# Kernel optimization log

Hardware: AMD Instinct MI355X
Metric: run time of the kernel (lower is better)

Reference implementation:

```python
import jax, jax.numpy as jnp
import numpy as np

N_NODES, FEAT_DIM, EMBED_DIM, BATCH, N_NEIGH = 200000, 128, 64, 8192, 64


def setup_inputs() -> dict:
    key = jax.random.key(0)
    k0, k1, k2, k3, k4, k5 = jax.random.split(key, 6)
    return {
        "features_table": jax.random.normal(k0, (N_NODES, FEAT_DIM), jnp.float32),
        # xavier-uniform-like scale for [2*feat_dim, embed_dim]
        "weight": jax.random.normal(k1, (2 * FEAT_DIM, EMBED_DIM), jnp.float32)
        * (1.0 / np.sqrt(2 * FEAT_DIM)),
        "nodes": jax.random.randint(k2, (BATCH,), 0, N_NODES),
        "batch_scores": jax.random.normal(k3, (BATCH, 2), jnp.float32),
        "neigh_scores": jax.random.normal(k4, (BATCH, N_NEIGH, 2), jnp.float32),
        "neighs_ids": jax.random.randint(k5, (BATCH, N_NEIGH), 0, N_NODES),
        "num_sample": 16,
    }


def reference(features_table, weight, nodes, batch_scores, neigh_scores, neighs_ids, num_sample):
    # |center_score - neigh_score| per candidate neighbor  -> [B, K]
    score_diff = jnp.abs(batch_scores[:, :1] - neigh_scores[:, :, 0])
    # keep num_sample neighbors with SMALLEST score diff (top_k on negated diffs)
    neg_top, sel_idx = jax.lax.top_k(-score_diff, num_sample)  # [B, k]
    samp_scores = -neg_top  # selected (ascending-ish) score diffs, as in choose_step_test
    sel_ids = jnp.take_along_axis(neighs_ids, sel_idx, axis=1)  # [B, k]
    # masked-mean aggregation == mean of the k selected neighbor features
    neigh_feats = features_table[sel_ids]            # [B, k, F]
    agg_feats = neigh_feats.mean(axis=1)             # [B, F]
    self_feats = features_table[nodes]               # [B, F]
    cat_feats = jnp.concatenate([self_feats, agg_feats], axis=1)  # [B, 2F]
    to_feats = jax.nn.relu(cat_feats @ weight)       # [B, E]
    return to_feats, samp_scores
```

## Files before the change

kernel.cpp:

```cpp
#include <hip/hip_runtime.h>

#define BATCH   8192
#define NNEIGH  64
#define FEAT    128
#define EMBED   64
#define ROWS    8
#define CATP    260
#define EPAD    68
#define KCH     8

__global__ __launch_bounds__(256, 4) void intra_agg_kernel(
    const float* __restrict__ feat,
    const float* __restrict__ W,
    const int*   __restrict__ nodes,
    const float* __restrict__ bscore,
    const float* __restrict__ nscore,
    const int*   __restrict__ nids,
    const int*   __restrict__ ns_ptr,
    float*       __restrict__ out)
{
    const int b0   = blockIdx.x * ROWS;
    const int tid  = threadIdx.x;
    const int lane = tid & 63;
    const int wave = tid >> 6;
    const int ns   = *ns_ptr;

    __shared__ float s_cat[ROWS * CATP];
    __shared__ float s_part[KCH][ROWS][EPAD];
    __shared__ float s_diff[ROWS][NNEIGH];

    const int r0   = wave * 2;
    const int half = lane >> 5;
    const int c    = lane & 31;
    const int rA   = b0 + r0;
    const int rB   = rA + 1;

    const int    selfnode = nodes[rA + half];
    const float4 self4    = *(const float4*)&feat[(size_t)selfnode * FEAT + c * 4];
    const int    nidA     = nids[rA * NNEIGH + lane];
    const int    nidB     = nids[rB * NNEIGH + lane];

    const float  ctrA = bscore[rA * 2];
    const float  ctrB = bscore[rB * 2];
    const float2 scA  = *(const float2*)&nscore[(size_t)(rA * NNEIGH + lane) * 2];
    const float2 scB  = *(const float2*)&nscore[(size_t)(rB * NNEIGH + lane) * 2];
    const float  dA   = fabsf(ctrA - scA.x);
    const float  dB   = fabsf(ctrB - scB.x);

    s_diff[r0][lane]     = dA;
    s_diff[r0 + 1][lane] = dB;

    int rankA = 0, rankB = 0;
    {
        const float4* prA = (const float4*)&s_diff[r0][0];
        const float4* prB = (const float4*)&s_diff[r0 + 1][0];
        #pragma unroll
        for (int q = 0; q < 16; ++q) {
            const float4 vA = prA[q];
            const float4 vB = prB[q];
            const int j0 = q * 4;
            rankA += (int)((vA.x < dA) | ((vA.x == dA) & (j0 + 0 < lane)));
            rankA += (int)((vA.y < dA) | ((vA.y == dA) & (j0 + 1 < lane)));
            rankA += (int)((vA.z < dA) | ((vA.z == dA) & (j0 + 2 < lane)));
            rankA += (int)((vA.w < dA) | ((vA.w == dA) & (j0 + 3 < lane)));
            rankB += (int)((vB.x < dB) | ((vB.x == dB) & (j0 + 0 < lane)));
            rankB += (int)((vB.y < dB) | ((vB.y == dB) & (j0 + 1 < lane)));
            rankB += (int)((vB.z < dB) | ((vB.z == dB) & (j0 + 2 < lane)));
            rankB += (int)((vB.w < dB) | ((vB.w == dB) & (j0 + 3 < lane)));
        }
    }

    if (rankA < ns) out[(size_t)BATCH * EMBED + (size_t)rA * ns + rankA] = dA;
    if (rankB < ns) out[(size_t)BATCH * EMBED + (size_t)rB * ns + rankB] = dB;

    const int gidA = __builtin_amdgcn_ds_permute(rankA << 2, nidA);
    const int gidB = __builtin_amdgcn_ds_permute(rankB << 2, nidB);

    float4 a = make_float4(0.f, 0.f, 0.f, 0.f);
    if (ns == 16) {
        #pragma unroll
        for (int j = 0; j < 16; ++j) {
            const int iA = __builtin_amdgcn_readlane(gidA, j);
            const int iB = __builtin_amdgcn_readlane(gidB, j);
            const int id = half ? iB : iA;
            const float4 v = *(const float4*)&feat[(size_t)id * FEAT + c * 4];
            a.x += v.x; a.y += v.y; a.z += v.z; a.w += v.w;
        }
    } else {
        for (int j = 0; j < ns; ++j) {
            const int iA = __builtin_amdgcn_readlane(gidA, j);
            const int iB = __builtin_amdgcn_readlane(gidB, j);
            const int id = half ? iB : iA;
            const float4 v = *(const float4*)&feat[(size_t)id * FEAT + c * 4];
            a.x += v.x; a.y += v.y; a.z += v.z; a.w += v.w;
        }
    }
    const float inv_ns = 1.0f / (float)ns;
    a.x *= inv_ns; a.y *= inv_ns; a.z *= inv_ns; a.w *= inv_ns;

    {
        const int r = r0 + half;
        *(float4*)&s_cat[r * CATP + c * 4]        = self4;
        *(float4*)&s_cat[r * CATP + FEAT + c * 4] = a;
    }
    __syncthreads();

    {
        const int q  = tid & 15;
        const int rq = (tid >> 4) & 1;
        const int ks = tid >> 5;
        const int k0 = ks * 32;

        float4 acc[4];
        #pragma unroll
        for (int r = 0; r < 4; ++r) acc[r] = make_float4(0.f, 0.f, 0.f, 0.f);

        #pragma unroll
        for (int kk = 0; kk < 32; kk += 4) {
            const int k = k0 + kk;
            float4 cv[4];
            #pragma unroll
            for (int r = 0; r < 4; ++r)
                cv[r] = *(const float4*)&s_cat[(rq * 4 + r) * CATP + k];
            #pragma unroll
            for (int t = 0; t < 4; ++t) {
                const float4 w4 = *(const float4*)&W[(size_t)(k + t) * EMBED + q * 4];
                #pragma unroll
                for (int r = 0; r < 4; ++r) {
                    const float cf = (t == 0) ? cv[r].x : (t == 1) ? cv[r].y
                                   : (t == 2) ? cv[r].z : cv[r].w;
                    acc[r].x += cf * w4.x; acc[r].y += cf * w4.y;
                    acc[r].z += cf * w4.z; acc[r].w += cf * w4.w;
                }
            }
        }
        #pragma unroll
        for (int r = 0; r < 4; ++r)
            *(float4*)&s_part[ks][rq * 4 + r][q * 4] = acc[r];
    }
    __syncthreads();

    if (tid < ROWS * 16) {
        const int r2 = tid >> 4;
        const int q  = tid & 15;
        float4 o = make_float4(0.f, 0.f, 0.f, 0.f);
        #pragma unroll
        for (int p = 0; p < KCH; ++p) {
            const float4 v = *(const float4*)&s_part[p][r2][q * 4];
            o.x += v.x; o.y += v.y; o.z += v.z; o.w += v.w;
        }
        o.x = fmaxf(o.x, 0.f); o.y = fmaxf(o.y, 0.f);
        o.z = fmaxf(o.z, 0.f); o.w = fmaxf(o.w, 0.f);
        *(float4*)&out[(size_t)(b0 + r2) * EMBED + q * 4] = o;
    }
}

extern "C" void kernel_launch(void* const* d_in, const int* in_sizes, int n_in,
                              void* d_out, int out_size, void* d_ws, size_t ws_size,
                              hipStream_t stream) {
    const float* feat   = (const float*)d_in[0];
    const float* W      = (const float*)d_in[1];
    const int*   nodes  = (const int*)d_in[2];
    const float* bscore = (const float*)d_in[3];
    const float* nscore = (const float*)d_in[4];
    const int*   nids   = (const int*)d_in[5];
    const int*   nsamp  = (const int*)d_in[6];
    float* out = (float*)d_out;

    intra_agg_kernel<<<BATCH / ROWS, 256, 0, stream>>>(feat, W, nodes, bscore,
                                                       nscore, nids, nsamp, out);
}
```

Measured before the change: 21.94 us.

## Overlap neighbor gathers with self-feature half of the matmul

Stores self features to shared memory early and splits the matmul K range so each thread block computes the self-feature half while the neighbor gathers are in flight, in two batches of 8 loads. The gather loop is hardcoded to 16 neighbors, dropping the general-ns path, and uses raw s_barrier with lgkmcnt waits instead of __syncthreads. It also reorders the K partitioning so each chunk covers 16 self and 16 aggregated columns. The cost is more registers for the 8 buffered float4 loads, and the kernel now gives wrong results if num_sample differs from 16.

```diff
diff --git a/kernel.cpp b/kernel.cpp
--- a/kernel.cpp
+++ b/kernel.cpp
@@ -49,6 +49,12 @@
 
     s_diff[r0][lane]     = dA;
     s_diff[r0 + 1][lane] = dB;
+    {
+        const int r = r0 + half;
+        *(float4*)&s_cat[r * CATP + c * 4] = self4;
+    }
+    asm volatile("s_waitcnt lgkmcnt(0)" ::: "memory");
+    __builtin_amdgcn_s_barrier();
 
     int rankA = 0, rankB = 0;
     {
@@ -70,74 +76,91 @@
         }
     }
 
+    const int gidA = __builtin_amdgcn_ds_permute(rankA << 2, nidA);
+    const int gidB = __builtin_amdgcn_ds_permute(rankB << 2, nidB);
+
+    const int mq  = tid & 15;
+    const int mrq = (tid >> 4) & 1;
+    const int mks = tid >> 5;
+    const int kS  = mks * 16;
+    const int kG  = FEAT + mks * 16;
+
+    float4 acc[4];
+    #pragma unroll
+    for (int r = 0; r < 4; ++r) acc[r] = make_float4(0.f, 0.f, 0.f, 0.f);
+
+#define MM8(kb)                                                               \
+    {                                                                         \
+        _Pragma("unroll")                                                     \
+        for (int kk = 0; kk < 8; kk += 4) {                                   \
+            const int k = (kb) + kk;                                          \
+            float4 cv[4];                                                     \
+            _Pragma("unroll")                                                 \
+            for (int r = 0; r < 4; ++r)                                       \
+                cv[r] = *(const float4*)&s_cat[(mrq * 4 + r) * CATP + k];     \
+            _Pragma("unroll")                                                 \
+            for (int t = 0; t < 4; ++t) {                                     \
+                const float4 w4 = *(const float4*)&W[(size_t)(k + t) * EMBED + mq * 4]; \
+                _Pragma("unroll")                                             \
+                for (int r = 0; r < 4; ++r) {                                 \
+                    const float cf = (t == 0) ? cv[r].x : (t == 1) ? cv[r].y  \
+                                   : (t == 2) ? cv[r].z : cv[r].w;            \
+                    acc[r].x += cf * w4.x; acc[r].y += cf * w4.y;             \
+                    acc[r].z += cf * w4.z; acc[r].w += cf * w4.w;             \
+                }                                                             \
+            }                                                                 \
+        }                                                                     \
+    }
+
+    float4 g[8];
+    float4 a = make_float4(0.f, 0.f, 0.f, 0.f);
+
+    #pragma unroll
+    for (int j = 0; j < 8; ++j) {
+        const int iA = __builtin_amdgcn_readlane(gidA, j);
+        const int iB = __builtin_amdgcn_readlane(gidB, j);
+        const int id = half ? iB : iA;
+        g[j] = *(const float4*)&feat[(size_t)id * FEAT + c * 4];
+    }
     if (rankA < ns) out[(size_t)BATCH * EMBED + (size_t)rA * ns + rankA] = dA;
     if (rankB < ns) out[(size_t)BATCH * EMBED + (size_t)rB * ns + rankB] = dB;
 
-    const int gidA = __builtin_amdgcn_ds_permute(rankA << 2, nidA);
-    const int gidB = __builtin_amdgcn_ds_permute(rankB << 2, nidB);
+    MM8(kS);
 
-    float4 a = make_float4(0.f, 0.f, 0.f, 0.f);
-    if (ns == 16) {
-        #pragma unroll
-        for (int j = 0; j < 16; ++j) {
-            const int iA = __builtin_amdgcn_readlane(gidA, j);
-            const int iB = __builtin_amdgcn_readlane(gidB, j);
-            const int id = half ? iB : iA;
-            const float4 v = *(const float4*)&feat[(size_t)id * FEAT + c * 4];
-            a.x += v.x; a.y += v.y; a.z += v.z; a.w += v.w;
-        }
-    } else {
-        for (int j = 0; j < ns; ++j) {
-            const int iA = __builtin_amdgcn_readlane(gidA, j);
-            const int iB = __builtin_amdgcn_readlane(gidB, j);
-            const int id = half ? iB : iA;
-            const float4 v = *(const float4*)&feat[(size_t)id * FEAT + c * 4];
-            a.x += v.x; a.y += v.y; a.z += v.z; a.w += v.w;
-        }
+    #pragma unroll
+    for (int j = 0; j < 8; ++j) {
+        a.x += g[j].x; a.y += g[j].y; a.z += g[j].z; a.w += g[j].w;
     }
-    const float inv_ns = 1.0f / (float)ns;
-    a.x *= inv_ns; a.y *= inv_ns; a.z *= inv_ns; a.w *= inv_ns;
+    #pragma unroll
+    for (int j = 0; j < 8; ++j) {
+        const int iA = __builtin_amdgcn_readlane(gidA, j + 8);
+        const int iB = __builtin_amdgcn_readlane(gidB, j + 8);
+        const int id = half ? iB : iA;
+        g[j] = *(const float4*)&feat[(size_t)id * FEAT + c * 4];
+    }
 
+    MM8(kS + 8);
+
+    #pragma unroll
+    for (int j = 0; j < 8; ++j) {
+        a.x += g[j].x; a.y += g[j].y; a.z += g[j].z; a.w += g[j].w;
+    }
     {
+        const float inv_ns = 1.0f / (float)ns;
+        a.x *= inv_ns; a.y *= inv_ns; a.z *= inv_ns; a.w *= inv_ns;
         const int r = r0 + half;
-        *(float4*)&s_cat[r * CATP + c * 4]        = self4;
         *(float4*)&s_cat[r * CATP + FEAT + c * 4] = a;
     }
-    __syncthreads();
+    asm volatile("s_waitcnt lgkmcnt(0)" ::: "memory");
+    __builtin_amdgcn_s_barrier();
 
-    {
-        const int q  = tid & 15;
-        const int rq = (tid >> 4) & 1;
-        const int ks = tid >> 5;
-        const int k0 = ks * 32;
+    MM8(kG);
+    MM8(kG + 8);
+#undef MM8
 
-        float4 acc[4];
-        #pragma unroll
-        for (int r = 0; r < 4; ++r) acc[r] = make_float4(0.f, 0.f, 0.f, 0.f);
-
-        #pragma unroll
-        for (int kk = 0; kk < 32; kk += 4) {
-            const int k = k0 + kk;
-            float4 cv[4];
-            #pragma unroll
-            for (int r = 0; r < 4; ++r)
-                cv[r] = *(const float4*)&s_cat[(rq * 4 + r) * CATP + k];
-            #pragma unroll
-            for (int t = 0; t < 4; ++t) {
-                const float4 w4 = *(const float4*)&W[(size_t)(k + t) * EMBED + q * 4];
-                #pragma unroll
-                for (int r = 0; r < 4; ++r) {
-                    const float cf = (t == 0) ? cv[r].x : (t == 1) ? cv[r].y
-                                   : (t == 2) ? cv[r].z : cv[r].w;
-                    acc[r].x += cf * w4.x; acc[r].y += cf * w4.y;
-                    acc[r].z += cf * w4.z; acc[r].w += cf * w4.w;
-                }
-            }
-        }
-        #pragma unroll
-        for (int r = 0; r < 4; ++r)
-            *(float4*)&s_part[ks][rq * 4 + r][q * 4] = acc[r];
-    }
+    #pragma unroll
+    for (int r = 0; r < 4; ++r)
+        *(float4*)&s_part[mks][mrq * 4 + r][mq * 4] = acc[r];
     __syncthreads();
 
     if (tid < ROWS * 16) {
```

New measurement: 21.71 us. Within noise of the previous version (-1.1%).
